# Performance work log

Hardware: AMD Instinct MI355X
Metric: run time of the kernel (lower is better)

The kernel has to match this reference:

```python
import jax, jax.numpy as jnp
import numpy as np

B, S, H, F, E, R, K = 2, 1024, 2048, 7168, 8, 32, 2


def setup_inputs() -> dict:
    key = jax.random.key(0)
    ks = jax.random.split(key, 12)
    sc = 0.02
    n = lambda k, shape, s: jax.random.normal(k, shape, dtype=jnp.float32) * s
    return {
        "hidden_states": n(ks[0], (B, S, H), 1.0),
        "Wg": n(ks[1], (E, H), sc),          # gate: Linear(H, E)
        "W1": n(ks[2], (F, H), sc),          # shared gate_proj
        "W2": n(ks[3], (H, F), sc),          # shared down_proj
        "W3": n(ks[4], (F, H), sc),          # shared up_proj
        "A1": n(ks[5], (E, R, H), sc),       # per-expert w1_a
        "B1": n(ks[6], (E, F, R), sc),       # per-expert w1_b
        "A2": n(ks[7], (E, R, F), sc),       # per-expert w2_a
        "B2": n(ks[8], (E, H, R), sc),       # per-expert w2_b
        "A3": n(ks[9], (E, R, H), sc),       # per-expert w3_a
        "B3": n(ks[10], (E, F, R), sc),      # per-expert w3_b
    }


def _gather_slot(a_all, e):
    # a_all: [T, E, r], e: [T] -> [T, r]
    return jnp.take_along_axis(a_all, e[:, None, None], axis=1)[:, 0]


def reference(hidden_states, Wg, W1, W2, W3, A1, B1, A2, B2, A3, B3):
    b, s, h = hidden_states.shape
    x = hidden_states.reshape(-1, h)                      # [T, H]
    nE = Wg.shape[0]
    logits = x @ Wg.T                                     # [T, E]
    probs = jax.nn.softmax(logits.astype(jnp.float32), axis=-1)
    rw, sel = jax.lax.top_k(probs, K)                     # [T, K]
    rw = (rw / rw.sum(axis=-1, keepdims=True)).astype(x.dtype)

    # Base projections are shared across experts -> compute once for all tokens.
    base1 = x @ W1.T                                      # [T, F]
    base3 = x @ W3.T                                      # [T, F]
    # Tiny per-expert LoRA down-projections for all tokens ([T, E, R]).
    a1_all = jnp.einsum('th,erh->ter', x, A1)
    a3_all = jnp.einsum('th,erh->ter', x, A3)

    out = jnp.zeros_like(x)
    for k in range(K):  # fixed small loop over top-k slots
        e = sel[:, k]                                     # [T]
        mask = jax.nn.one_hot(e, nE, dtype=x.dtype)       # [T, E]
        a1 = _gather_slot(a1_all, e)                      # [T, R]
        a3 = _gather_slot(a3_all, e)
        lora1 = jnp.einsum('ter,efr->tf', mask[:, :, None] * a1[:, None, :], B1)
        lora3 = jnp.einsum('ter,efr->tf', mask[:, :, None] * a3[:, None, :], B3)
        x1 = base1 + lora1
        x3 = base3 + lora3
        x2 = jax.nn.silu(x1) * x3                         # [T, F]
        down = x2 @ W2.T                                  # [T, H]
        a2_all = jnp.einsum('tf,erf->ter', x2, A2)        # [T, E, R]
        a2 = _gather_slot(a2_all, e)
        lora2 = jnp.einsum('ter,ehr->th', mask[:, :, None] * a2[:, None, :], B2)
        out = out + (down + lora2) * rw[:, k:k+1]
    return out.reshape(b, s, h)
```

## Files before the change

### kernel.cpp

```cpp
#include <hip/hip_runtime.h>

typedef unsigned short u16;
typedef unsigned int u32;
typedef __attribute__((ext_vector_type(4))) float f32x4;
typedef __attribute__((ext_vector_type(8))) short short8;

constexpr int TT = 2048;
constexpr int HH = 2048;
constexpr int FF = 7168;
constexpr int RR = 32;
constexpr int KT = 2;
constexpr int NA1 = FF + 256;
constexpr int NA2 = HH + 256;

__device__ __forceinline__ float bf2f(u16 v) {
  union { u32 u; float f; } w; w.u = ((u32)v) << 16; return w.f;
}
__device__ __forceinline__ u16 f2bf(float f) {
  union { float f; u32 u; } w; w.f = f;
  u32 u = w.u;
  return (u16)((u + 0x7FFFu + ((u >> 16) & 1u)) >> 16);
}

__device__ __forceinline__ void gload16(const u16* g, u16* l) {
  __builtin_amdgcn_global_load_lds(
      (__attribute__((address_space(1))) void*)g,
      (__attribute__((address_space(3))) void*)l, 16, 0, 0);
}

__device__ __forceinline__ void bar_mem() { asm volatile("s_barrier" ::: "memory"); }
__device__ __forceinline__ void lgk0() { asm volatile("s_waitcnt lgkmcnt(0)" ::: "memory"); }
template <int N>
__device__ __forceinline__ void vmw() { asm volatile("s_waitcnt vmcnt(%0)" :: "n"(N) : "memory"); }

__global__ __launch_bounds__(256) void cvt_kernel(
    const float* __restrict__ src, u16* __restrict__ dst, int n4) {
  int stride = gridDim.x * 256;
  for (int i = blockIdx.x * 256 + threadIdx.x; i < n4; i += stride) {
    float4 v = ((const float4*)src)[i];
    ushort4 o;
    o.x = f2bf(v.x); o.y = f2bf(v.y); o.z = f2bf(v.z); o.w = f2bf(v.w);
    ((ushort4*)dst)[i] = o;
  }
}

__global__ __launch_bounds__(256) void repackB_kernel(
    const float* __restrict__ B, u16* __restrict__ Bm, int Fdim) {
  int n = Fdim * 256;
  int stride = gridDim.x * 256;
  for (int i = blockIdx.x * 256 + threadIdx.x; i < n; i += stride) {
    int f = i >> 8, c = i & 255, e = c >> 5, r = c & 31;
    Bm[i] = f2bf(B[((size_t)e * Fdim + f) * RR + r]);
  }
}

__global__ __launch_bounds__(64) void gating_kernel(
    const float* __restrict__ X, const float* __restrict__ Wg,
    int* __restrict__ sel, float* __restrict__ rw) {
  int t = blockIdx.x;
  int lane = threadIdx.x;
  const float* x = X + (size_t)t * HH;
  float acc[8] = {};
  for (int h = lane; h < HH; h += 64) {
    float xv = x[h];
#pragma unroll
    for (int e = 0; e < 8; e++) acc[e] += xv * Wg[e * HH + h];
  }
#pragma unroll
  for (int e = 0; e < 8; e++)
    for (int off = 32; off; off >>= 1) acc[e] += __shfl_down(acc[e], off);
  if (lane == 0) {
    int b0 = 0; float l0 = acc[0];
    for (int e = 1; e < 8; e++) if (acc[e] > l0) { l0 = acc[e]; b0 = e; }
    int b1 = -1; float l1 = 0.f;
    for (int e = 0; e < 8; e++) {
      if (e == b0) continue;
      if (b1 < 0 || acc[e] > l1) { l1 = acc[e]; b1 = e; }
    }
    float p = 1.f / (1.f + __expf(l1 - l0));
    sel[t * 2 + 0] = b0; sel[t * 2 + 1] = b1;
    rw[t * 2 + 0] = p;   rw[t * 2 + 1] = 1.f - p;
  }
}

__device__ __forceinline__ void stageH(const u16* g, int stride, int row0, int k0,
                                       u16* l) {
  const int tid = threadIdx.x;
#pragma unroll
  for (int j = 0; j < 2; ++j) {
    int c = (j << 9) + tid;
    int row = c >> 3, c8 = c & 7;
    int sc = ((c8 ^ (row & 7)) << 3);
    gload16(g + (size_t)(row0 + row) * stride + (k0 + sc), l + c * 8);
  }
}

#define RD_A(buf, mo)                                                         \
  _Pragma("unroll") for (int j = 0; j < 4; ++j)                               \
  _Pragma("unroll") for (int ks = 0; ks < 2; ++ks) {                          \
    int row = wmw + (mo + j) * 16 + r15;                                      \
    a[j * 2 + ks] = *(const short8*)((buf) + row * 64 +                       \
                                     (((ks * 4 + q) ^ (row & 7)) << 3));      \
  }
#define RD_B(buf, reg, no)                                                    \
  _Pragma("unroll") for (int n = 0; n < 2; ++n)                               \
  _Pragma("unroll") for (int ks = 0; ks < 2; ++ks) {                          \
    int row = wnw + (no + n) * 16 + r15;                                      \
    reg[n * 2 + ks] = *(const short8*)((buf) + row * 64 +                     \
                                       (((ks * 4 + q) ^ (row & 7)) << 3));    \
  }
#define MMQ(mo, reg, no)                                                      \
  _Pragma("unroll") for (int m = 0; m < 4; ++m)                               \
  _Pragma("unroll") for (int n = 0; n < 2; ++n)                               \
  _Pragma("unroll") for (int ks = 0; ks < 2; ++ks)                            \
    acc[mo + m][no + n] = __builtin_amdgcn_mfma_f32_16x16x32_bf16(            \
        a[m * 2 + ks], reg[n * 2 + ks], acc[mo + m][no + n], 0, 0, 0);

__global__ __launch_bounds__(512, 2) void gemm256(
    const u16* A0, const u16* A1p, const u16* B0, const u16* B1p,
    u16* Cb0, u16* Cb1, int N, int Kd) {
  const u16* A  = blockIdx.z ? A1p : A0;
  const u16* Bm = blockIdx.z ? B1p : B0;
  u16* Cb       = blockIdx.z ? Cb1 : Cb0;

  __shared__ __align__(16) u16 S[81920];
  u16* Acur  = S;
  u16* Anext = S + 16384;
  u16* Afree = S + 32768;
  u16* B0b   = S + 49152;
  u16* B1b   = S + 65536;

  const int gx = gridDim.x, gy = gridDim.y;
  const int nwg = gx * gy;
  const int orig = blockIdx.y * gx + blockIdx.x;
  const int wg = (orig & 7) * (nwg >> 3) + (orig >> 3);
  const int tn = (wg / gy) * 256;
  const int tm = (wg % gy) * 256;

  const int tid = threadIdx.x;
  const int lane = tid & 63, wave = tid >> 6;
  const int wmw = (wave >> 2) * 128;
  const int wnw = (wave & 3) * 64;
  const int r15 = lane & 15, q = lane >> 4;

  f32x4 acc[8][4] = {};
  short8 a[8], bl[4], bh[4];

  const int nIter = Kd >> 7;

  stageH(A,  Kd, tm,       0,  Acur);
  stageH(A,  Kd, tm + 128, 0,  Acur + 8192);
  stageH(Bm, Kd, tn,       0,  B0b);
  stageH(Bm, Kd, tn + 128, 0,  B0b + 8192);
  stageH(A,  Kd, tm,       64, Anext);
  stageH(A,  Kd, tm + 128, 64, Anext + 8192);
  stageH(Bm, Kd, tn,       64, B1b);
  stageH(Bm, Kd, tn + 128, 64, B1b + 8192);
  vmw<8>();
  bar_mem();

  for (int it = 0; it < nIter; ++it) {
    const bool st = (it + 1 < nIter);
    const int k2 = (2 * it + 2) << 6;
    const int k3 = (2 * it + 3) << 6;

    RD_A(Acur, 0) RD_B(B0b, bl, 0)
    if (st) stageH(A, Kd, tm, k2, Afree);
    bar_mem(); lgk0();
    __builtin_amdgcn_s_setprio(1); MMQ(0, bl, 0) __builtin_amdgcn_s_setprio(0);
    bar_mem();
    RD_B(B0b, bh, 2)
    if (st) stageH(A, Kd, tm + 128, k2, Afree + 8192);
    bar_mem(); lgk0();
    __builtin_amdgcn_s_setprio(1); MMQ(0, bh, 2) __builtin_amdgcn_s_setprio(0);
    bar_mem();
    RD_A(Acur, 4)
    if (st) stageH(Bm, Kd, tn, k2, B0b);
    bar_mem(); lgk0();
    __builtin_amdgcn_s_setprio(1); MMQ(4, bh, 2) __builtin_amdgcn_s_setprio(0);
    bar_mem();
    if (st) stageH(Bm, Kd, tn + 128, k2, B0b + 8192);
    bar_mem();
    __builtin_amdgcn_s_setprio(1); MMQ(4, bl, 0) __builtin_amdgcn_s_setprio(0);
    if (st) vmw<8>(); else vmw<0>();
    bar_mem();

    RD_A(Anext, 0) RD_B(B1b, bl, 0)
    if (st) stageH(A, Kd, tm, k3, Acur);
    bar_mem(); lgk0();
    __builtin_amdgcn_s_setprio(1); MMQ(0, bl, 0) __builtin_amdgcn_s_setprio(0);
    bar_mem();
    RD_B(B1b, bh, 2)
    if (st) stageH(A, Kd, tm + 128, k3, Acur + 8192);
    bar_mem(); lgk0();
    __builtin_amdgcn_s_setprio(1); MMQ(0, bh, 2) __builtin_amdgcn_s_setprio(0);
    bar_mem();
    RD_A(Anext, 4)
    if (st) stageH(Bm, Kd, tn, k3, B1b);
    bar_mem(); lgk0();
    __builtin_amdgcn_s_setprio(1); MMQ(4, bh, 2) __builtin_amdgcn_s_setprio(0);
    bar_mem();
    if (st) stageH(Bm, Kd, tn + 128, k3, B1b + 8192);
    bar_mem();
    __builtin_amdgcn_s_setprio(1); MMQ(4, bl, 0) __builtin_amdgcn_s_setprio(0);
    if (st) vmw<8>();
    bar_mem();

    u16* tmp = Afree; Afree = Anext; Anext = Acur; Acur = tmp;
  }

#pragma unroll
  for (int m = 0; m < 8; ++m)
#pragma unroll
    for (int n = 0; n < 4; ++n)
#pragma unroll
      for (int i = 0; i < 4; ++i) {
        int r = tm + wmw + m * 16 + q * 4 + i;
        int cc = tn + wnw + n * 16 + r15;
        Cb[(size_t)r * N + cc] = f2bf(acc[m][n][i]);
      }
}

__global__ __launch_bounds__(256) void gemm_bt(
    const u16* A0, const u16* A1p,
    const u16* B0, const u16* B1p,
    u16* Cb0, u16* Cb1, float* Cf0, float* Cf1,
    int N, int Kd, int out_bf16) {
  const u16* A  = blockIdx.z ? A1p : A0;
  const u16* Bm = blockIdx.z ? B1p : B0;
  u16* Cb       = blockIdx.z ? Cb1 : Cb0;
  float* Cf     = blockIdx.z ? Cf1 : Cf0;

  __shared__ __align__(16) u16 As[128 * 64];
  __shared__ __align__(16) u16 Bs[128 * 64];

  int tid = threadIdx.x;
  int tn = blockIdx.x * 128;
  int tm = blockIdx.y * 128;
  int lane = tid & 63;
  int wave = tid >> 6;
  int wm = (wave >> 1) * 64, wn = (wave & 1) * 64;
  const int r15 = lane & 15, q = lane >> 4;

  f32x4 acc[4][4] = {};

  for (int k0 = 0; k0 < Kd; k0 += 64) {
#pragma unroll
    for (int it = 0; it < 4; it++) {
      int c = it * 256 + tid;
      int row = c >> 3, c8 = c & 7;
      int scol = ((c8 ^ (row & 7)) << 3);
      gload16(A + (size_t)(tm + row) * Kd + (k0 + scol), As + c * 8);
      gload16(Bm + (size_t)(tn + row) * Kd + (k0 + scol), Bs + c * 8);
    }
    __syncthreads();
#pragma unroll
    for (int kk = 0; kk < 2; kk++) {
      short8 af[4], bfr[4];
#pragma unroll
      for (int mi = 0; mi < 4; mi++) {
        int row = wm + mi * 16 + r15;
        int kc = (kk * 4 + q) ^ (row & 7);
        af[mi] = *(const short8*)(As + row * 64 + kc * 8);
      }
#pragma unroll
      for (int ni = 0; ni < 4; ni++) {
        int row = wn + ni * 16 + r15;
        int kc = (kk * 4 + q) ^ (row & 7);
        bfr[ni] = *(const short8*)(Bs + row * 64 + kc * 8);
      }
#pragma unroll
      for (int mi = 0; mi < 4; mi++)
#pragma unroll
        for (int ni = 0; ni < 4; ni++)
          acc[mi][ni] = __builtin_amdgcn_mfma_f32_16x16x32_bf16(af[mi], bfr[ni], acc[mi][ni], 0, 0, 0);
    }
    __syncthreads();
  }
#pragma unroll
  for (int mi = 0; mi < 4; mi++)
#pragma unroll
    for (int ni = 0; ni < 4; ni++)
#pragma unroll
      for (int i = 0; i < 4; i++) {
        int r = tm + wm + mi * 16 + q * 4 + i;
        int cc = tn + wn + ni * 16 + r15;
        float v = acc[mi][ni][i];
        if (out_bf16) Cb[(size_t)r * N + cc] = f2bf(v);
        else          Cf[(size_t)r * N + cc] = v;
      }
}

__global__ __launch_bounds__(256) void mask13_kernel(
    const u16* __restrict__ Y1, const u16* __restrict__ Y3,
    const int* __restrict__ sel, u16* __restrict__ ah1, u16* __restrict__ ah3) {
  int tk = blockIdx.x;
  int t = tk >> 1;
  int e = sel[tk] & 7;
  int c = threadIdx.x;
  bool in = (c >> 5) == e;
  ah1[(size_t)tk * 256 + c] = in ? Y1[(size_t)t * NA1 + FF + c] : (u16)0;
  ah3[(size_t)tk * 256 + c] = in ? Y3[(size_t)t * NA1 + FF + c] : (u16)0;
}

__global__ __launch_bounds__(256) void mask2_kernel(
    const u16* __restrict__ down_aug, const int* __restrict__ sel,
    u16* __restrict__ ah2) {
  int tk = blockIdx.x;
  int t = tk >> 1, k = tk & 1;
  int e = sel[tk] & 7;
  int c = threadIdx.x;
  ah2[(size_t)tk * 256 + c] =
      ((c >> 5) == e) ? down_aug[((size_t)k * TT + t) * NA2 + HH + c] : (u16)0;
}

__global__ __launch_bounds__(256) void lora_silu_kernel(
    const u16* __restrict__ ah1, const u16* __restrict__ ah3,
    const u16* __restrict__ Bm1, const u16* __restrict__ Bm3,
    const u16* __restrict__ Y1, const u16* __restrict__ Y3,
    u16* __restrict__ X2) {
  __shared__ __align__(16) u16 Bs1[128 * 64];
  __shared__ __align__(16) u16 Bs3[128 * 64];
  int tid = threadIdx.x;
  int tn = blockIdx.x * 128;
  int tm = blockIdx.y * 128;
  int lane = tid & 63, wave = tid >> 6;
  int wm = (wave >> 1) * 64, wn = (wave & 1) * 64;
  const int r15 = lane & 15, q = lane >> 4;

  f32x4 acc1[4][4] = {}, acc3[4][4] = {};

  for (int k0 = 0; k0 < 256; k0 += 64) {
#pragma unroll
    for (int it = 0; it < 4; it++) {
      int c = it * 256 + tid;
      int row = c >> 3, c8 = c & 7;
      int scol = ((c8 ^ (row & 7)) << 3);
      gload16(Bm1 + (size_t)(tn + row) * 256 + (k0 + scol), Bs1 + c * 8);
      gload16(Bm3 + (size_t)(tn + row) * 256 + (k0 + scol), Bs3 + c * 8);
    }
    __syncthreads();
#pragma unroll
    for (int kk = 0; kk < 2; kk++) {
      short8 a1f[4], a3f[4], b1f[4], b3f[4];
#pragma unroll
      for (int mi = 0; mi < 4; mi++) {
        int row = tm + wm + mi * 16 + r15;
        size_t o = (size_t)row * 256 + k0 + (kk * 4 + q) * 8;
        a1f[mi] = *(const short8*)(ah1 + o);
        a3f[mi] = *(const short8*)(ah3 + o);
      }
#pragma unroll
      for (int ni = 0; ni < 4; ni++) {
        int row = wn + ni * 16 + r15;
        int kc = (kk * 4 + q) ^ (row & 7);
        b1f[ni] = *(const short8*)(Bs1 + row * 64 + kc * 8);
        b3f[ni] = *(const short8*)(Bs3 + row * 64 + kc * 8);
      }
#pragma unroll
      for (int mi = 0; mi < 4; mi++)
#pragma unroll
        for (int ni = 0; ni < 4; ni++) {
          acc1[mi][ni] = __builtin_amdgcn_mfma_f32_16x16x32_bf16(a1f[mi], b1f[ni], acc1[mi][ni], 0, 0, 0);
          acc3[mi][ni] = __builtin_amdgcn_mfma_f32_16x16x32_bf16(a3f[mi], b3f[ni], acc3[mi][ni], 0, 0, 0);
        }
    }
    __syncthreads();
  }
#pragma unroll
  for (int mi = 0; mi < 4; mi++)
#pragma unroll
    for (int ni = 0; ni < 4; ni++)
#pragma unroll
      for (int i = 0; i < 4; i++) {
        int row = tm + wm + mi * 16 + q * 4 + i;
        int f = tn + wn + ni * 16 + r15;
        int t = row >> 1, k = row & 1;
        float x1 = bf2f(Y1[(size_t)t * NA1 + f]) + acc1[mi][ni][i];
        float x3 = bf2f(Y3[(size_t)t * NA1 + f]) + acc3[mi][ni][i];
        float sig = 1.f / (1.f + __expf(-x1));
        X2[((size_t)k * TT + t) * FF + f] = f2bf(x1 * sig * x3);
      }
}

__global__ __launch_bounds__(256) void final_kernel(
    const u16* __restrict__ down_aug, const float* __restrict__ L2b,
    const float* __restrict__ rw, float* __restrict__ out) {
  int t = blockIdx.x;
  float r0 = rw[t * 2], r1 = rw[t * 2 + 1];
  int h = threadIdx.x * 8;
  short8 d0v = *(const short8*)(down_aug + (size_t)t * NA2 + h);
  short8 d1v = *(const short8*)(down_aug + ((size_t)TT + t) * NA2 + h);
  const float* l0p = L2b + (size_t)(t * 2) * HH + h;
  const float* l1p = L2b + (size_t)(t * 2 + 1) * HH + h;
  f32x4 l0a = *(const f32x4*)(l0p),     l0b = *(const f32x4*)(l0p + 4);
  f32x4 l1a = *(const f32x4*)(l1p),     l1b = *(const f32x4*)(l1p + 4);
  f32x4 oa, ob;
#pragma unroll
  for (int j = 0; j < 4; j++) {
    oa[j] = r0 * (bf2f((u16)d0v[j])     + l0a[j]) + r1 * (bf2f((u16)d1v[j])     + l1a[j]);
    ob[j] = r0 * (bf2f((u16)d0v[j + 4]) + l0b[j]) + r1 * (bf2f((u16)d1v[j + 4]) + l1b[j]);
  }
  float* op = out + (size_t)t * HH + h;
  *(f32x4*)(op)     = oa;
  *(f32x4*)(op + 4) = ob;
}

extern "C" void kernel_launch(void* const* d_in, const int* in_sizes, int n_in,
                              void* d_out, int out_size, void* d_ws, size_t ws_size,
                              hipStream_t stream) {
  if (n_in < 11) return;
  const float* X  = (const float*)d_in[0];
  const float* Wg = (const float*)d_in[1];
  const float* W1 = (const float*)d_in[2];
  const float* W2 = (const float*)d_in[3];
  const float* W3 = (const float*)d_in[4];
  const float* A1 = (const float*)d_in[5];
  const float* B1 = (const float*)d_in[6];
  const float* A2 = (const float*)d_in[7];
  const float* B2 = (const float*)d_in[8];
  const float* A3 = (const float*)d_in[9];
  const float* B3 = (const float*)d_in[10];
  float* out = (float*)d_out;

  char* ws = (char*)d_ws;
  size_t off = 0;
  auto take = [&](size_t bytes) -> void* {
    void* p = ws + off;
    off += (bytes + 255) & ~(size_t)255;
    return p;
  };
  u16*   Xb     = (u16*)take((size_t)TT * HH * 2);
  u16*   W1augb = (u16*)take((size_t)NA1 * HH * 2);
  u16*   W3augb = (u16*)take((size_t)NA1 * HH * 2);
  u16*   W2augb = (u16*)take((size_t)NA2 * FF * 2);
  u16*   Bm1    = (u16*)take((size_t)FF * 256 * 2);
  u16*   Bm3    = (u16*)take((size_t)FF * 256 * 2);
  u16*   Bm2    = (u16*)take((size_t)HH * 256 * 2);
  u16*   Y1aug  = (u16*)take((size_t)TT * NA1 * 2);
  u16*   Y3aug  = (u16*)take((size_t)TT * NA1 * 2);
  u16*   ah1    = (u16*)take((size_t)TT * KT * 256 * 2);
  u16*   ah3    = (u16*)take((size_t)TT * KT * 256 * 2);
  u16*   ah2    = (u16*)take((size_t)TT * KT * 256 * 2);
  u16*   X2     = (u16*)take((size_t)KT * TT * FF * 2);
  int*   sel    = (int*)take((size_t)TT * KT * 4);
  float* rw     = (float*)take((size_t)TT * KT * 4);
  if (off > ws_size) return;
  u16*   down_aug = W1augb;
  float* L2b      = (float*)W3augb;

  cvt_kernel<<<1024, 256, 0, stream>>>(X,  Xb, TT * HH / 4);
  cvt_kernel<<<1024, 256, 0, stream>>>(W1, W1augb, FF * HH / 4);
  cvt_kernel<<<1024, 256, 0, stream>>>(A1, W1augb + (size_t)FF * HH, 256 * HH / 4);
  cvt_kernel<<<1024, 256, 0, stream>>>(W3, W3augb, FF * HH / 4);
  cvt_kernel<<<1024, 256, 0, stream>>>(A3, W3augb + (size_t)FF * HH, 256 * HH / 4);
  cvt_kernel<<<1024, 256, 0, stream>>>(W2, W2augb, HH * FF / 4);
  cvt_kernel<<<1024, 256, 0, stream>>>(A2, W2augb + (size_t)HH * FF, 256 * FF / 4);
  repackB_kernel<<<1024, 256, 0, stream>>>(B1, Bm1, FF);
  repackB_kernel<<<1024, 256, 0, stream>>>(B3, Bm3, FF);
  repackB_kernel<<<1024, 256, 0, stream>>>(B2, Bm2, HH);
  gating_kernel<<<TT, 64, 0, stream>>>(X, Wg, sel, rw);

  gemm256<<<dim3(NA1 / 256, TT / 256, 2), 512, 0, stream>>>(
      Xb, Xb, W1augb, W3augb, Y1aug, Y3aug, NA1, HH);
  mask13_kernel<<<TT * KT, 256, 0, stream>>>(Y1aug, Y3aug, sel, ah1, ah3);
  lora_silu_kernel<<<dim3(FF / 128, TT * KT / 128), 256, 0, stream>>>(
      ah1, ah3, Bm1, Bm3, Y1aug, Y3aug, X2);
  gemm256<<<dim3(NA2 / 256, TT / 256, 2), 512, 0, stream>>>(
      X2, X2 + (size_t)TT * FF, W2augb, W2augb,
      down_aug, down_aug + (size_t)TT * NA2, NA2, FF);
  mask2_kernel<<<TT * KT, 256, 0, stream>>>(down_aug, sel, ah2);
  gemm_bt<<<dim3(HH / 128, TT * KT / 128, 1), 256, 0, stream>>>(
      ah2, ah2, Bm2, Bm2, nullptr, nullptr, L2b, L2b, HH, 256, 0);
  final_kernel<<<TT, 256, 0, stream>>>(down_aug, L2b, rw, out);
}
```

Baseline: 701.3 us.

## Fuse fp32-to-bf16 conversions into one launch and keep LoRA B tiles resident

Replaces seven separate conversion launches with a single prep kernel that walks all source arrays through one flattened index range. The LoRA+SiLU kernel is restructured to load the full 128x256 B1/B3 slices (128 KB of LDS) once per block with 512 threads, then loop over four 128-row M tiles. This drops repeated B reloads and per-k-step barriers. It trades away occupancy, since each block now uses 128 KB of LDS, and the grid has four times fewer blocks. The prep kernel also adds branchy index dispatch.

```diff
diff --git a/kernel.cpp b/kernel.cpp
--- a/kernel.cpp
+++ b/kernel.cpp
@@ -33,14 +33,34 @@
 template <int N>
 __device__ __forceinline__ void vmw() { asm volatile("s_waitcnt vmcnt(%0)" :: "n"(N) : "memory"); }
 
-__global__ __launch_bounds__(256) void cvt_kernel(
-    const float* __restrict__ src, u16* __restrict__ dst, int n4) {
+__global__ __launch_bounds__(256) void prep_kernel(
+    const float* __restrict__ X,  u16* __restrict__ Xb,
+    const float* __restrict__ W1, const float* __restrict__ A1, u16* __restrict__ W1augb,
+    const float* __restrict__ W3, const float* __restrict__ A3, u16* __restrict__ W3augb,
+    const float* __restrict__ W2, const float* __restrict__ A2, u16* __restrict__ W2augb) {
+  constexpr int n0 = TT * HH / 4;
+  constexpr int n1 = FF * HH / 4;
+  constexpr int n2 = 256 * HH / 4;
+  constexpr int n3 = FF * HH / 4;
+  constexpr int n4 = 256 * HH / 4;
+  constexpr int n5 = HH * FF / 4;
+  constexpr int n6 = 256 * FF / 4;
+  constexpr int c0 = n0, c1 = c0 + n1, c2 = c1 + n2, c3 = c2 + n3,
+                c4 = c3 + n4, c5 = c4 + n5, c6 = c5 + n6;
   int stride = gridDim.x * 256;
-  for (int i = blockIdx.x * 256 + threadIdx.x; i < n4; i += stride) {
-    float4 v = ((const float4*)src)[i];
+  for (int i = blockIdx.x * 256 + threadIdx.x; i < c6; i += stride) {
+    const float* src; u16* dst; int j;
+    if (i < c0)      { src = X;  dst = Xb;                          j = i; }
+    else if (i < c1) { src = W1; dst = W1augb;                      j = i - c0; }
+    else if (i < c2) { src = A1; dst = W1augb + (size_t)FF * HH;    j = i - c1; }
+    else if (i < c3) { src = W3; dst = W3augb;                      j = i - c2; }
+    else if (i < c4) { src = A3; dst = W3augb + (size_t)FF * HH;    j = i - c3; }
+    else if (i < c5) { src = W2; dst = W2augb;                      j = i - c4; }
+    else             { src = A2; dst = W2augb + (size_t)HH * FF;    j = i - c5; }
+    float4 v = ((const float4*)src)[j];
     ushort4 o;
     o.x = f2bf(v.x); o.y = f2bf(v.y); o.z = f2bf(v.z); o.w = f2bf(v.w);
-    ((ushort4*)dst)[i] = o;
+    ((ushort4*)dst)[j] = o;
   }
 }
 
@@ -314,73 +334,77 @@
       ((c >> 5) == e) ? down_aug[((size_t)k * TT + t) * NA2 + HH + c] : (u16)0;
 }
 
-__global__ __launch_bounds__(256) void lora_silu_kernel(
+__global__ __launch_bounds__(512) void lora_silu2(
     const u16* __restrict__ ah1, const u16* __restrict__ ah3,
     const u16* __restrict__ Bm1, const u16* __restrict__ Bm3,
     const u16* __restrict__ Y1, const u16* __restrict__ Y3,
     u16* __restrict__ X2) {
-  __shared__ __align__(16) u16 Bs1[128 * 64];
-  __shared__ __align__(16) u16 Bs3[128 * 64];
-  int tid = threadIdx.x;
-  int tn = blockIdx.x * 128;
-  int tm = blockIdx.y * 128;
-  int lane = tid & 63, wave = tid >> 6;
-  int wm = (wave >> 1) * 64, wn = (wave & 1) * 64;
+  __shared__ __align__(16) u16 Bs[2][4][128 * 64];
+  const int tid = threadIdx.x;
+  const int tn = blockIdx.x * 128;
+  const int lane = tid & 63, wave = tid >> 6;
+  const int wm = (wave >> 2) * 64;
+  const int wn = (wave & 3) * 32;
   const int r15 = lane & 15, q = lane >> 4;
 
-  f32x4 acc1[4][4] = {}, acc3[4][4] = {};
-
-  for (int k0 = 0; k0 < 256; k0 += 64) {
-#pragma unroll
-    for (int it = 0; it < 4; it++) {
-      int c = it * 256 + tid;
-      int row = c >> 3, c8 = c & 7;
-      int scol = ((c8 ^ (row & 7)) << 3);
-      gload16(Bm1 + (size_t)(tn + row) * 256 + (k0 + scol), Bs1 + c * 8);
-      gload16(Bm3 + (size_t)(tn + row) * 256 + (k0 + scol), Bs3 + c * 8);
+  for (int c = 0; c < 4; ++c) {
+#pragma unroll
+    for (int j = 0; j < 2; ++j) {
+      int idx = (j << 9) + tid;
+      int row = idx >> 3, c8 = idx & 7;
+      int sc = ((c8 ^ (row & 7)) << 3);
+      gload16(Bm1 + (size_t)(tn + row) * 256 + (c * 64 + sc), &Bs[0][c][idx * 8]);
+      gload16(Bm3 + (size_t)(tn + row) * 256 + (c * 64 + sc), &Bs[1][c][idx * 8]);
     }
-    __syncthreads();
-#pragma unroll
-    for (int kk = 0; kk < 2; kk++) {
-      short8 a1f[4], a3f[4], b1f[4], b3f[4];
-#pragma unroll
-      for (int mi = 0; mi < 4; mi++) {
-        int row = tm + wm + mi * 16 + r15;
-        size_t o = (size_t)row * 256 + k0 + (kk * 4 + q) * 8;
-        a1f[mi] = *(const short8*)(ah1 + o);
-        a3f[mi] = *(const short8*)(ah3 + o);
+  }
+  vmw<0>();
+  __syncthreads();
+
+  for (int t = 0; t < 4; ++t) {
+    const int tm = (blockIdx.y * 4 + t) * 128;
+    f32x4 acc1[4][2] = {}, acc3[4][2] = {};
+    for (int c = 0; c < 4; ++c) {
+#pragma unroll
+      for (int kk = 0; kk < 2; ++kk) {
+        short8 a1f[4], a3f[4], b1f[2], b3f[2];
+#pragma unroll
+        for (int mi = 0; mi < 4; ++mi) {
+          int row = tm + wm + mi * 16 + r15;
+          size_t o = (size_t)row * 256 + c * 64 + (kk * 4 + q) * 8;
+          a1f[mi] = *(const short8*)(ah1 + o);
+          a3f[mi] = *(const short8*)(ah3 + o);
+        }
+#pragma unroll
+        for (int ni = 0; ni < 2; ++ni) {
+          int row = wn + ni * 16 + r15;
+          int kc = (kk * 4 + q) ^ (row & 7);
+          b1f[ni] = *(const short8*)(&Bs[0][c][row * 64 + kc * 8]);
+          b3f[ni] = *(const short8*)(&Bs[1][c][row * 64 + kc * 8]);
+        }
+#pragma unroll
+        for (int mi = 0; mi < 4; ++mi)
+#pragma unroll
+          for (int ni = 0; ni < 2; ++ni) {
+            acc1[mi][ni] = __builtin_amdgcn_mfma_f32_16x16x32_bf16(a1f[mi], b1f[ni], acc1[mi][ni], 0, 0, 0);
+            acc3[mi][ni] = __builtin_amdgcn_mfma_f32_16x16x32_bf16(a3f[mi], b3f[ni], acc3[mi][ni], 0, 0, 0);
+          }
       }
-#pragma unroll
-      for (int ni = 0; ni < 4; ni++) {
-        int row = wn + ni * 16 + r15;
-        int kc = (kk * 4 + q) ^ (row & 7);
-        b1f[ni] = *(const short8*)(Bs1 + row * 64 + kc * 8);
-        b3f[ni] = *(const short8*)(Bs3 + row * 64 + kc * 8);
-      }
-#pragma unroll
-      for (int mi = 0; mi < 4; mi++)
-#pragma unroll
-        for (int ni = 0; ni < 4; ni++) {
-          acc1[mi][ni] = __builtin_amdgcn_mfma_f32_16x16x32_bf16(a1f[mi], b1f[ni], acc1[mi][ni], 0, 0, 0);
-          acc3[mi][ni] = __builtin_amdgcn_mfma_f32_16x16x32_bf16(a3f[mi], b3f[ni], acc3[mi][ni], 0, 0, 0);
+    }
+#pragma unroll
+    for (int mi = 0; mi < 4; ++mi)
+#pragma unroll
+      for (int ni = 0; ni < 2; ++ni)
+#pragma unroll
+        for (int i = 0; i < 4; ++i) {
+          int row = tm + wm + mi * 16 + q * 4 + i;
+          int f = tn + wn + ni * 16 + r15;
+          int t2 = row >> 1, k = row & 1;
+          float x1 = bf2f(Y1[(size_t)t2 * NA1 + f]) + acc1[mi][ni][i];
+          float x3 = bf2f(Y3[(size_t)t2 * NA1 + f]) + acc3[mi][ni][i];
+          float sig = 1.f / (1.f + __expf(-x1));
+          X2[((size_t)k * TT + t2) * FF + f] = f2bf(x1 * sig * x3);
         }
-    }
-    __syncthreads();
-  }
-#pragma unroll
-  for (int mi = 0; mi < 4; mi++)
-#pragma unroll
-    for (int ni = 0; ni < 4; ni++)
-#pragma unroll
-      for (int i = 0; i < 4; i++) {
-        int row = tm + wm + mi * 16 + q * 4 + i;
-        int f = tn + wn + ni * 16 + r15;
-        int t = row >> 1, k = row & 1;
-        float x1 = bf2f(Y1[(size_t)t * NA1 + f]) + acc1[mi][ni][i];
-        float x3 = bf2f(Y3[(size_t)t * NA1 + f]) + acc3[mi][ni][i];
-        float sig = 1.f / (1.f + __expf(-x1));
-        X2[((size_t)k * TT + t) * FF + f] = f2bf(x1 * sig * x3);
-      }
+  }
 }
 
 __global__ __launch_bounds__(256) void final_kernel(
@@ -449,13 +473,8 @@
   u16*   down_aug = W1augb;
   float* L2b      = (float*)W3augb;
 
-  cvt_kernel<<<1024, 256, 0, stream>>>(X,  Xb, TT * HH / 4);
-  cvt_kernel<<<1024, 256, 0, stream>>>(W1, W1augb, FF * HH / 4);
-  cvt_kernel<<<1024, 256, 0, stream>>>(A1, W1augb + (size_t)FF * HH, 256 * HH / 4);
-  cvt_kernel<<<1024, 256, 0, stream>>>(W3, W3augb, FF * HH / 4);
-  cvt_kernel<<<1024, 256, 0, stream>>>(A3, W3augb + (size_t)FF * HH, 256 * HH / 4);
-  cvt_kernel<<<1024, 256, 0, stream>>>(W2, W2augb, HH * FF / 4);
-  cvt_kernel<<<1024, 256, 0, stream>>>(A2, W2augb + (size_t)HH * FF, 256 * FF / 4);
+  prep_kernel<<<2048, 256, 0, stream>>>(X, Xb, W1, A1, W1augb, W3, A3, W3augb,
+                                        W2, A2, W2augb);
   repackB_kernel<<<1024, 256, 0, stream>>>(B1, Bm1, FF);
   repackB_kernel<<<1024, 256, 0, stream>>>(B3, Bm3, FF);
   repackB_kernel<<<1024, 256, 0, stream>>>(B2, Bm2, HH);
@@ -464,7 +483,7 @@
   gemm256<<<dim3(NA1 / 256, TT / 256, 2), 512, 0, stream>>>(
       Xb, Xb, W1augb, W3augb, Y1aug, Y3aug, NA1, HH);
   mask13_kernel<<<TT * KT, 256, 0, stream>>>(Y1aug, Y3aug, sel, ah1, ah3);
-  lora_silu_kernel<<<dim3(FF / 128, TT * KT / 128), 256, 0, stream>>>(
+  lora_silu2<<<dim3(FF / 128, TT * KT / 128 / 4), 512, 0, stream>>>(
       ah1, ah3, Bm1, Bm3, Y1aug, Y3aug, X2);
   gemm256<<<dim3(NA2 / 256, TT / 256, 2), 512, 0, stream>>>(
       X2, X2 + (size_t)TT * FF, W2augb, W2augb,
```

Result: slower. 753.2 us (+7.4%).
